# Optimization experiments

Measured on AMD Instinct MI355X. Metric: run time of the kernel, lower is better.

Reference implementation:

```python
import jax, jax.numpy as jnp
import numpy as np

B, S, H, I, E, K = 4, 1024, 1024, 768, 8, 2


def setup_inputs() -> dict:
    key = jax.random.key(0)
    ks = jax.random.split(key, 6)
    return {
        "hidden_states": jax.random.normal(ks[0], (B, S, H), dtype=jnp.float32),
        "routing_weights": jax.random.uniform(ks[1], (B, S, K), dtype=jnp.float32),
        "selected_experts": jax.random.randint(ks[2], (B, S, K), 0, E, dtype=jnp.int64),
        "gate_weight": jax.random.normal(ks[3], (E, I, H), dtype=jnp.float32) * 0.02,
        "up_weight": jax.random.normal(ks[4], (E, I, H), dtype=jnp.float32) * 0.02,
        "down_weight": jax.random.normal(ks[5], (E, H, I), dtype=jnp.float32) * 0.02,
    }


def reference(hidden_states, routing_weights, selected_experts, gate_weight, up_weight, down_weight):
    b, s, h = hidden_states.shape
    x = hidden_states.reshape(-1, h)                    # [T, H]
    T = x.shape[0]
    k = selected_experts.shape[-1]
    rw = routing_weights.astype(x.dtype).reshape(T, k)  # [T, K]
    se = selected_experts.reshape(T, k)                 # [T, K]
    e_total = gate_weight.shape[0]
    # combine[t, e] = sum of routing weights of slots of token t routed to expert e
    # (equivalent to the original per-slot dispatch + weighted scatter-add combine)
    combine = jnp.zeros((T, e_total), dtype=x.dtype).at[jnp.arange(T)[:, None], se].add(rw)
    out = jnp.zeros_like(x)
    for e in range(e_total):  # small fixed expert count
        g = x @ gate_weight[e].T                        # [T, I]
        u = x @ up_weight[e].T                          # [T, I]
        y = (jax.nn.silu(g) * u) @ down_weight[e].T     # [T, H]
        out = out + combine[:, e:e + 1] * y
    return out.reshape(b, s, h)
```

## Files before the change

kernel.cpp:

```cpp
#include <hip/hip_runtime.h>
#include <hip/hip_bf16.h>

typedef __attribute__((ext_vector_type(8))) short bf16x8;
typedef __attribute__((ext_vector_type(4))) float f32x4;

#define T_TOK 4096
#define HDIM  1024
#define IDIM  768
#define NEXP  8
#define TOPK  2
#define NSLOT (T_TOK * TOPK)

#define BM  128
#define BN  64
#define BKS 64

#define NX4 (T_TOK * HDIM / 4)
#define NW4 (NEXP * IDIM * HDIM / 4)

__device__ __forceinline__ ushort f2bf(float f) {
  union { __hip_bfloat16 h; ushort u; } cv;
  cv.h = __float2bfloat16(f);
  return cv.u;
}
__device__ __forceinline__ float bf2f(ushort u) {
  union { float f; uint v; } cv; cv.v = ((uint)u) << 16; return cv.f;
}

__device__ __forceinline__ void gload_lds16(const ushort* g, ushort* l) {
  __builtin_amdgcn_global_load_lds(
      (const __attribute__((address_space(1))) void*)g,
      (__attribute__((address_space(3))) void*)l, 16, 0, 0);
}

__global__ void cvt_all(const float* __restrict__ hs, const float* __restrict__ gw,
                        const float* __restrict__ uw, const float* __restrict__ dw,
                        ushort* __restrict__ xb, ushort* __restrict__ gwb,
                        ushort* __restrict__ uwb, ushort* __restrict__ dwb) {
  int i = blockIdx.x * blockDim.x + threadIdx.x;
  const float* src; ushort* dst; int off;
  if (i < NX4) { src = hs; dst = xb; off = i; }
  else {
    int j = i - NX4;
    if (j < NW4)            { src = gw; dst = gwb; off = j; }
    else if (j < 2 * NW4)   { src = uw; dst = uwb; off = j - NW4; }
    else                    { src = dw; dst = dwb; off = j - 2 * NW4; }
  }
  float4 v = reinterpret_cast<const float4*>(src)[off];
  ushort4 o;
  o.x = f2bf(v.x); o.y = f2bf(v.y); o.z = f2bf(v.z); o.w = f2bf(v.w);
  reinterpret_cast<ushort4*>(dst)[off] = o;
}

__global__ void route_kernel(const int* __restrict__ sel, int* __restrict__ counts,
                             int* __restrict__ toklist) {
  int slot = blockIdx.x * blockDim.x + threadIdx.x;
  if (slot >= NSLOT) return;
  int e = sel[slot];
  int idx = atomicAdd(&counts[e], 1);
  toklist[e * NSLOT + idx] = slot;
}

__launch_bounds__(256, 2)
__global__ void gemm_gateup(const ushort* __restrict__ xb,
                            const ushort* __restrict__ gwb,
                            const ushort* __restrict__ uwb,
                            const int* __restrict__ counts,
                            const int* __restrict__ toklist,
                            ushort* __restrict__ act) {
  const int e = blockIdx.z;
  const int cnt = counts[e];
  const int m0 = blockIdx.y * BM;
  if (m0 >= cnt) return;
  const int n0 = blockIdx.x * BN;

  __shared__ __align__(16) ushort As[2][BM * BKS];
  __shared__ __align__(16) ushort Bgs[2][BN * BKS];
  __shared__ __align__(16) ushort Bus[2][BN * BKS];

  const int tid = threadIdx.x;
  const int wave = tid >> 6, lane = tid & 63;
  const int wm = wave >> 1, wn = wave & 1;
  const int lrow = lane & 15, lk16 = lane >> 4;
  const int rseg = lane >> 3;
  const int ksrc = (lane & 7) ^ rseg;

  int arow[4];
  #pragma unroll
  for (int i = 0; i < 4; ++i) {
    int entry = m0 + wave * 32 + i * 8 + rseg;
    int s = (entry < cnt) ? toklist[e * NSLOT + entry] : 0;
    arow[i] = s >> 1;
  }

  const ushort* gB = gwb + (size_t)e * IDIM * HDIM + (size_t)n0 * HDIM;
  const ushort* uB = uwb + (size_t)e * IDIM * HDIM + (size_t)n0 * HDIM;

  f32x4 accg[4][2], accu[4][2];
  const f32x4 fzero = {0.f, 0.f, 0.f, 0.f};
  #pragma unroll
  for (int a = 0; a < 4; ++a)
    #pragma unroll
    for (int b = 0; b < 2; ++b) { accg[a][b] = fzero; accu[a][b] = fzero; }

  auto stage = [&](int buf, int k0) {
    #pragma unroll
    for (int i = 0; i < 4; ++i) {
      int seg = wave * 4 + i;
      gload_lds16(xb + (size_t)arow[i] * HDIM + k0 + ksrc * 8, &As[buf][seg * 512]);
    }
    #pragma unroll
    for (int i = 0; i < 2; ++i) {
      int seg = wave * 2 + i;
      int br = seg * 8 + rseg;
      gload_lds16(gB + (size_t)br * HDIM + k0 + ksrc * 8, &Bgs[buf][seg * 512]);
      gload_lds16(uB + (size_t)br * HDIM + k0 + ksrc * 8, &Bus[buf][seg * 512]);
    }
  };

  auto compute = [&](int buf) {
    #pragma unroll
    for (int ksub = 0; ksub < 2; ++ksub) {
      bf16x8 aF[4], bgF[2], buF[2];
      const int chunk = ksub * 4 + lk16;
      #pragma unroll
      for (int mi = 0; mi < 4; ++mi) {
        int r = wm * 64 + mi * 16 + lrow;
        aF[mi] = *reinterpret_cast<const bf16x8*>(&As[buf][r * 64 + ((chunk ^ (r & 7)) & 7) * 8]);
      }
      #pragma unroll
      for (int ni = 0; ni < 2; ++ni) {
        int r = wn * 32 + ni * 16 + lrow;
        bgF[ni] = *reinterpret_cast<const bf16x8*>(&Bgs[buf][r * 64 + ((chunk ^ (r & 7)) & 7) * 8]);
        buF[ni] = *reinterpret_cast<const bf16x8*>(&Bus[buf][r * 64 + ((chunk ^ (r & 7)) & 7) * 8]);
      }
      #pragma unroll
      for (int mi = 0; mi < 4; ++mi)
        #pragma unroll
        for (int ni = 0; ni < 2; ++ni) {
          accg[mi][ni] = __builtin_amdgcn_mfma_f32_16x16x32_bf16(aF[mi], bgF[ni], accg[mi][ni], 0, 0, 0);
          accu[mi][ni] = __builtin_amdgcn_mfma_f32_16x16x32_bf16(aF[mi], buF[ni], accu[mi][ni], 0, 0, 0);
        }
    }
  };

  stage(0, 0);
  __syncthreads();
  #pragma unroll 1
  for (int t = 0; t < HDIM / BKS; t += 2) {
    if (t + 1 < HDIM / BKS) stage(1, (t + 1) * BKS);
    compute(0);
    __syncthreads();
    if (t + 2 < HDIM / BKS) stage(0, (t + 2) * BKS);
    compute(1);
    __syncthreads();
  }

  const int lcol = lane & 15;
  const int lrb = (lane >> 4) * 4;
  #pragma unroll
  for (int mi = 0; mi < 4; ++mi)
    #pragma unroll
    for (int j = 0; j < 4; ++j) {
      int row = wm * 64 + mi * 16 + lrb + j;
      int entry = m0 + row;
      if (entry >= cnt) continue;
      int slot = toklist[e * NSLOT + entry];
      #pragma unroll
      for (int ni = 0; ni < 2; ++ni) {
        int col = n0 + wn * 32 + ni * 16 + lcol;
        float g = accg[mi][ni][j];
        float u = accu[mi][ni][j];
        float y = (g / (1.0f + __expf(-g))) * u;
        act[(size_t)slot * IDIM + col] = f2bf(y);
      }
    }
}

__launch_bounds__(256, 3)
__global__ void gemm_down(const ushort* __restrict__ act,
                          const ushort* __restrict__ dwb,
                          const int* __restrict__ counts,
                          const int* __restrict__ toklist,
                          ushort* __restrict__ yact) {
  const int e = blockIdx.z;
  const int cnt = counts[e];
  const int m0 = blockIdx.y * BM;
  if (m0 >= cnt) return;
  const int n0 = blockIdx.x * BN;

  __shared__ __align__(16) ushort As[2][BM * BKS];
  __shared__ __align__(16) ushort Bs[2][BN * BKS];

  const int tid = threadIdx.x;
  const int wave = tid >> 6, lane = tid & 63;
  const int wm = wave >> 1, wn = wave & 1;
  const int lrow = lane & 15, lk16 = lane >> 4;
  const int rseg = lane >> 3;
  const int ksrc = (lane & 7) ^ rseg;

  int arow[4];
  #pragma unroll
  for (int i = 0; i < 4; ++i) {
    int entry = m0 + wave * 32 + i * 8 + rseg;
    arow[i] = (entry < cnt) ? toklist[e * NSLOT + entry] : 0;
  }

  const ushort* dB = dwb + (size_t)e * HDIM * IDIM + (size_t)n0 * IDIM;

  f32x4 acc[4][2];
  const f32x4 fzero = {0.f, 0.f, 0.f, 0.f};
  #pragma unroll
  for (int a = 0; a < 4; ++a)
    #pragma unroll
    for (int b = 0; b < 2; ++b) acc[a][b] = fzero;

  auto stage = [&](int buf, int k0) {
    #pragma unroll
    for (int i = 0; i < 4; ++i) {
      int seg = wave * 4 + i;
      gload_lds16(act + (size_t)arow[i] * IDIM + k0 + ksrc * 8, &As[buf][seg * 512]);
    }
    #pragma unroll
    for (int i = 0; i < 2; ++i) {
      int seg = wave * 2 + i;
      int br = seg * 8 + rseg;
      gload_lds16(dB + (size_t)br * IDIM + k0 + ksrc * 8, &Bs[buf][seg * 512]);
    }
  };

  auto compute = [&](int buf) {
    #pragma unroll
    for (int ksub = 0; ksub < 2; ++ksub) {
      bf16x8 aF[4], bF[2];
      const int chunk = ksub * 4 + lk16;
      #pragma unroll
      for (int mi = 0; mi < 4; ++mi) {
        int r = wm * 64 + mi * 16 + lrow;
        aF[mi] = *reinterpret_cast<const bf16x8*>(&As[buf][r * 64 + ((chunk ^ (r & 7)) & 7) * 8]);
      }
      #pragma unroll
      for (int ni = 0; ni < 2; ++ni) {
        int r = wn * 32 + ni * 16 + lrow;
        bF[ni] = *reinterpret_cast<const bf16x8*>(&Bs[buf][r * 64 + ((chunk ^ (r & 7)) & 7) * 8]);
      }
      #pragma unroll
      for (int mi = 0; mi < 4; ++mi)
        #pragma unroll
        for (int ni = 0; ni < 2; ++ni)
          acc[mi][ni] = __builtin_amdgcn_mfma_f32_16x16x32_bf16(aF[mi], bF[ni], acc[mi][ni], 0, 0, 0);
    }
  };

  stage(0, 0);
  __syncthreads();
  #pragma unroll 1
  for (int t = 0; t < IDIM / BKS; t += 2) {
    if (t + 1 < IDIM / BKS) stage(1, (t + 1) * BKS);
    compute(0);
    __syncthreads();
    if (t + 2 < IDIM / BKS) stage(0, (t + 2) * BKS);
    compute(1);
    __syncthreads();
  }

  const int lcol = lane & 15;
  const int lrb = (lane >> 4) * 4;
  #pragma unroll
  for (int mi = 0; mi < 4; ++mi)
    #pragma unroll
    for (int j = 0; j < 4; ++j) {
      int row = wm * 64 + mi * 16 + lrb + j;
      int entry = m0 + row;
      if (entry >= cnt) continue;
      int slot = toklist[e * NSLOT + entry];
      #pragma unroll
      for (int ni = 0; ni < 2; ++ni) {
        int col = n0 + wn * 32 + ni * 16 + lcol;
        yact[(size_t)slot * HDIM + col] = f2bf(acc[mi][ni][j]);
      }
    }
}

__global__ void combine_kernel(const ushort* __restrict__ yact, const float* __restrict__ rw,
                               float* __restrict__ out) {
  int i = blockIdx.x * blockDim.x + threadIdx.x;
  int t = i >> 7;
  int h0 = (i & 127) << 3;
  const bf16x8 y0 = *reinterpret_cast<const bf16x8*>(yact + (size_t)(2 * t) * HDIM + h0);
  const bf16x8 y1 = *reinterpret_cast<const bf16x8*>(yact + (size_t)(2 * t + 1) * HDIM + h0);
  float w0 = rw[2 * t], w1 = rw[2 * t + 1];
  float o[8];
  #pragma unroll
  for (int j = 0; j < 8; ++j)
    o[j] = w0 * bf2f((ushort)y0[j]) + w1 * bf2f((ushort)y1[j]);
  float4* op = reinterpret_cast<float4*>(out + (size_t)t * HDIM + h0);
  op[0] = make_float4(o[0], o[1], o[2], o[3]);
  op[1] = make_float4(o[4], o[5], o[6], o[7]);
}

extern "C" void kernel_launch(void* const* d_in, const int* in_sizes, int n_in,
                              void* d_out, int out_size, void* d_ws, size_t ws_size,
                              hipStream_t stream) {
  const float* hs = (const float*)d_in[0];
  const float* rw = (const float*)d_in[1];
  const int*   se = (const int*)d_in[2];
  const float* gw = (const float*)d_in[3];
  const float* uw = (const float*)d_in[4];
  const float* dw = (const float*)d_in[5];
  float* out = (float*)d_out;

  char* base = (char*)d_ws;
  ushort* xb      = (ushort*)(base + 0);
  ushort* gwb     = (ushort*)(base + 8388608);
  ushort* uwb     = (ushort*)(base + 20971520);
  ushort* dwb     = (ushort*)(base + 33554432);
  ushort* act     = (ushort*)(base + 46137344);
  ushort* yact    = (ushort*)(base + 8388608);
  int*    toklist = (int*)(base + 58720256);
  int*    counts  = (int*)(base + 58982400);

  hipMemsetAsync(counts, 0, 256, stream);

  int total4 = NX4 + 3 * NW4;
  cvt_all<<<(total4 + 255) / 256, 256, 0, stream>>>(hs, gw, uw, dw, xb, gwb, uwb, dwb);
  route_kernel<<<NSLOT / 256, 256, 0, stream>>>(se, counts, toklist);
  gemm_gateup<<<dim3(IDIM / BN, NSLOT / BM, NEXP), 256, 0, stream>>>(xb, gwb, uwb, counts, toklist, act);
  gemm_down<<<dim3(HDIM / BN, NSLOT / BM, NEXP), 256, 0, stream>>>(act, dwb, counts, toklist, yact);
  combine_kernel<<<T_TOK * HDIM / 8 / 256, 256, 0, stream>>>(yact, rw, out);
}
```

Baseline: 253.1 us.

## Halve K-tile to 32, raise occupancy, and flatten grid with expert-interleaved block order

The K-step of both grouped GEMMs drops from 64 to 32, which halves LDS use per block. Launch bounds rise to 3 and 4 blocks per CU to match. The staging and swizzle are rewritten for 32-wide rows, with one 16-byte load per lane per tile. The 3D grid becomes a 1D grid with the expert as the fastest-varying index, so blocks of different experts run together and the early-exit empty blocks are spread out. The cost is twice as many K iterations and barriers, plus more register pressure from the tighter launch bounds.

```diff
diff --git a/kernel.cpp b/kernel.cpp
--- a/kernel.cpp
+++ b/kernel.cpp
@@ -13,7 +13,7 @@
 
 #define BM  128
 #define BN  64
-#define BKS 64
+#define BKS 32
 
 #define NX4 (T_TOK * HDIM / 4)
 #define NW4 (NEXP * IDIM * HDIM / 4)
@@ -61,18 +61,22 @@
   toklist[e * NSLOT + idx] = slot;
 }
 
-__launch_bounds__(256, 2)
+
+__launch_bounds__(256, 3)
 __global__ void gemm_gateup(const ushort* __restrict__ xb,
                             const ushort* __restrict__ gwb,
                             const ushort* __restrict__ uwb,
                             const int* __restrict__ counts,
                             const int* __restrict__ toklist,
                             ushort* __restrict__ act) {
-  const int e = blockIdx.z;
+  const int b = blockIdx.x;
+  const int e = b & 7;
+  const int r = b >> 3;
+  const int nt = r % 12, mt = r / 12;
   const int cnt = counts[e];
-  const int m0 = blockIdx.y * BM;
+  const int m0 = mt * BM;
   if (m0 >= cnt) return;
-  const int n0 = blockIdx.x * BN;
+  const int n0 = nt * BN;
 
   __shared__ __align__(16) ushort As[2][BM * BKS];
   __shared__ __align__(16) ushort Bgs[2][BN * BKS];
@@ -82,66 +86,55 @@
   const int wave = tid >> 6, lane = tid & 63;
   const int wm = wave >> 1, wn = wave & 1;
   const int lrow = lane & 15, lk16 = lane >> 4;
-  const int rseg = lane >> 3;
-  const int ksrc = (lane & 7) ^ rseg;
-
-  int arow[4];
-  #pragma unroll
-  for (int i = 0; i < 4; ++i) {
-    int entry = m0 + wave * 32 + i * 8 + rseg;
-    int s = (entry < cnt) ? toklist[e * NSLOT + entry] : 0;
-    arow[i] = s >> 1;
-  }
-
-  const ushort* gB = gwb + (size_t)e * IDIM * HDIM + (size_t)n0 * HDIM;
-  const ushort* uB = uwb + (size_t)e * IDIM * HDIM + (size_t)n0 * HDIM;
+  const int rl = lane >> 2;
+  const int gck = ((lane & 3) ^ ((lane >> 3) & 3)) << 3;
+
+  const int ent0 = m0 + wave * 16 + rl;
+  const int ent1 = ent0 + 64;
+  const int arow0 = (ent0 < cnt) ? (toklist[e * NSLOT + ent0] >> 1) : 0;
+  const int arow1 = (ent1 < cnt) ? (toklist[e * NSLOT + ent1] >> 1) : 0;
+  const int brow = wave * 16 + rl;
+
+  const ushort* aP0 = xb + (size_t)arow0 * HDIM + gck;
+  const ushort* aP1 = xb + (size_t)arow1 * HDIM + gck;
+  const ushort* gP = gwb + (size_t)e * IDIM * HDIM + (size_t)(n0 + brow) * HDIM + gck;
+  const ushort* uP = uwb + (size_t)e * IDIM * HDIM + (size_t)(n0 + brow) * HDIM + gck;
 
   f32x4 accg[4][2], accu[4][2];
   const f32x4 fzero = {0.f, 0.f, 0.f, 0.f};
   #pragma unroll
   for (int a = 0; a < 4; ++a)
     #pragma unroll
-    for (int b = 0; b < 2; ++b) { accg[a][b] = fzero; accu[a][b] = fzero; }
+    for (int c = 0; c < 2; ++c) { accg[a][c] = fzero; accu[a][c] = fzero; }
 
   auto stage = [&](int buf, int k0) {
-    #pragma unroll
-    for (int i = 0; i < 4; ++i) {
-      int seg = wave * 4 + i;
-      gload_lds16(xb + (size_t)arow[i] * HDIM + k0 + ksrc * 8, &As[buf][seg * 512]);
-    }
-    #pragma unroll
-    for (int i = 0; i < 2; ++i) {
-      int seg = wave * 2 + i;
-      int br = seg * 8 + rseg;
-      gload_lds16(gB + (size_t)br * HDIM + k0 + ksrc * 8, &Bgs[buf][seg * 512]);
-      gload_lds16(uB + (size_t)br * HDIM + k0 + ksrc * 8, &Bus[buf][seg * 512]);
-    }
+    gload_lds16(aP0 + k0, &As[buf][wave * 512]);
+    gload_lds16(aP1 + k0, &As[buf][(wave + 4) * 512]);
+    gload_lds16(gP + k0, &Bgs[buf][wave * 512]);
+    gload_lds16(uP + k0, &Bus[buf][wave * 512]);
   };
 
+  const int swzc = ((lk16 ^ ((lrow >> 1) & 3)) << 3);
   auto compute = [&](int buf) {
-    #pragma unroll
-    for (int ksub = 0; ksub < 2; ++ksub) {
-      bf16x8 aF[4], bgF[2], buF[2];
-      const int chunk = ksub * 4 + lk16;
-      #pragma unroll
-      for (int mi = 0; mi < 4; ++mi) {
-        int r = wm * 64 + mi * 16 + lrow;
-        aF[mi] = *reinterpret_cast<const bf16x8*>(&As[buf][r * 64 + ((chunk ^ (r & 7)) & 7) * 8]);
-      }
+    bf16x8 aF[4], bgF[2], buF[2];
+    #pragma unroll
+    for (int mi = 0; mi < 4; ++mi) {
+      int rr = wm * 64 + mi * 16 + lrow;
+      aF[mi] = *reinterpret_cast<const bf16x8*>(&As[buf][rr * 32 + swzc]);
+    }
+    #pragma unroll
+    for (int ni = 0; ni < 2; ++ni) {
+      int rr = wn * 32 + ni * 16 + lrow;
+      bgF[ni] = *reinterpret_cast<const bf16x8*>(&Bgs[buf][rr * 32 + swzc]);
+      buF[ni] = *reinterpret_cast<const bf16x8*>(&Bus[buf][rr * 32 + swzc]);
+    }
+    #pragma unroll
+    for (int mi = 0; mi < 4; ++mi)
       #pragma unroll
       for (int ni = 0; ni < 2; ++ni) {
-        int r = wn * 32 + ni * 16 + lrow;
-        bgF[ni] = *reinterpret_cast<const bf16x8*>(&Bgs[buf][r * 64 + ((chunk ^ (r & 7)) & 7) * 8]);
-        buF[ni] = *reinterpret_cast<const bf16x8*>(&Bus[buf][r * 64 + ((chunk ^ (r & 7)) & 7) * 8]);
+        accg[mi][ni] = __builtin_amdgcn_mfma_f32_16x16x32_bf16(aF[mi], bgF[ni], accg[mi][ni], 0, 0, 0);
+        accu[mi][ni] = __builtin_amdgcn_mfma_f32_16x16x32_bf16(aF[mi], buF[ni], accu[mi][ni], 0, 0, 0);
       }
-      #pragma unroll
-      for (int mi = 0; mi < 4; ++mi)
-        #pragma unroll
-        for (int ni = 0; ni < 2; ++ni) {
-          accg[mi][ni] = __builtin_amdgcn_mfma_f32_16x16x32_bf16(aF[mi], bgF[ni], accg[mi][ni], 0, 0, 0);
-          accu[mi][ni] = __builtin_amdgcn_mfma_f32_16x16x32_bf16(aF[mi], buF[ni], accu[mi][ni], 0, 0, 0);
-        }
-    }
   };
 
   stage(0, 0);
@@ -177,17 +170,20 @@
     }
 }
 
-__launch_bounds__(256, 3)
+__launch_bounds__(256, 4)
 __global__ void gemm_down(const ushort* __restrict__ act,
                           const ushort* __restrict__ dwb,
                           const int* __restrict__ counts,
                           const int* __restrict__ toklist,
                           ushort* __restrict__ yact) {
-  const int e = blockIdx.z;
+  const int b = blockIdx.x;
+  const int e = b & 7;
+  const int r = b >> 3;
+  const int nt = r & 15, mt = r >> 4;
   const int cnt = counts[e];
-  const int m0 = blockIdx.y * BM;
+  const int m0 = mt * BM;
   if (m0 >= cnt) return;
-  const int n0 = blockIdx.x * BN;
+  const int n0 = nt * BN;
 
   __shared__ __align__(16) ushort As[2][BM * BKS];
   __shared__ __align__(16) ushort Bs[2][BN * BKS];
@@ -196,60 +192,50 @@
   const int wave = tid >> 6, lane = tid & 63;
   const int wm = wave >> 1, wn = wave & 1;
   const int lrow = lane & 15, lk16 = lane >> 4;
-  const int rseg = lane >> 3;
-  const int ksrc = (lane & 7) ^ rseg;
-
-  int arow[4];
-  #pragma unroll
-  for (int i = 0; i < 4; ++i) {
-    int entry = m0 + wave * 32 + i * 8 + rseg;
-    arow[i] = (entry < cnt) ? toklist[e * NSLOT + entry] : 0;
-  }
-
-  const ushort* dB = dwb + (size_t)e * HDIM * IDIM + (size_t)n0 * IDIM;
+  const int rl = lane >> 2;
+  const int gck = ((lane & 3) ^ ((lane >> 3) & 3)) << 3;
+
+  const int ent0 = m0 + wave * 16 + rl;
+  const int ent1 = ent0 + 64;
+  const int arow0 = (ent0 < cnt) ? toklist[e * NSLOT + ent0] : 0;
+  const int arow1 = (ent1 < cnt) ? toklist[e * NSLOT + ent1] : 0;
+  const int brow = wave * 16 + rl;
+
+  const ushort* aP0 = act + (size_t)arow0 * IDIM + gck;
+  const ushort* aP1 = act + (size_t)arow1 * IDIM + gck;
+  const ushort* dP = dwb + (size_t)e * HDIM * IDIM + (size_t)(n0 + brow) * IDIM + gck;
 
   f32x4 acc[4][2];
   const f32x4 fzero = {0.f, 0.f, 0.f, 0.f};
   #pragma unroll
   for (int a = 0; a < 4; ++a)
     #pragma unroll
-    for (int b = 0; b < 2; ++b) acc[a][b] = fzero;
+    for (int c = 0; c < 2; ++c) acc[a][c] = fzero;
 
   auto stage = [&](int buf, int k0) {
-    #pragma unroll
-    for (int i = 0; i < 4; ++i) {
-      int seg = wave * 4 + i;
-      gload_lds16(act + (size_t)arow[i] * IDIM + k0 + ksrc * 8, &As[buf][seg * 512]);
-    }
-    #pragma unroll
-    for (int i = 0; i < 2; ++i) {
-      int seg = wave * 2 + i;
-      int br = seg * 8 + rseg;
-      gload_lds16(dB + (size_t)br * IDIM + k0 + ksrc * 8, &Bs[buf][seg * 512]);
-    }
+    gload_lds16(aP0 + k0, &As[buf][wave * 512]);
+    gload_lds16(aP1 + k0, &As[buf][(wave + 4) * 512]);
+    gload_lds16(dP + k0, &Bs[buf][wave * 512]);
   };
 
+  const int swzc = ((lk16 ^ ((lrow >> 1) & 3)) << 3);
   auto compute = [&](int buf) {
-    #pragma unroll
-    for (int ksub = 0; ksub < 2; ++ksub) {
-      bf16x8 aF[4], bF[2];
-      const int chunk = ksub * 4 + lk16;
+    bf16x8 aF[4], bF[2];
+    #pragma unroll
+    for (int mi = 0; mi < 4; ++mi) {
+      int rr = wm * 64 + mi * 16 + lrow;
+      aF[mi] = *reinterpret_cast<const bf16x8*>(&As[buf][rr * 32 + swzc]);
+    }
+    #pragma unroll
+    for (int ni = 0; ni < 2; ++ni) {
+      int rr = wn * 32 + ni * 16 + lrow;
+      bF[ni] = *reinterpret_cast<const bf16x8*>(&Bs[buf][rr * 32 + swzc]);
+    }
+    #pragma unroll
+    for (int mi = 0; mi < 4; ++mi)
       #pragma unroll
-      for (int mi = 0; mi < 4; ++mi) {
-        int r = wm * 64 + mi * 16 + lrow;
-        aF[mi] = *reinterpret_cast<const bf16x8*>(&As[buf][r * 64 + ((chunk ^ (r & 7)) & 7) * 8]);
-      }
-      #pragma unroll
-      for (int ni = 0; ni < 2; ++ni) {
-        int r = wn * 32 + ni * 16 + lrow;
-        bF[ni] = *reinterpret_cast<const bf16x8*>(&Bs[buf][r * 64 + ((chunk ^ (r & 7)) & 7) * 8]);
-      }
-      #pragma unroll
-      for (int mi = 0; mi < 4; ++mi)
-        #pragma unroll
-        for (int ni = 0; ni < 2; ++ni)
-          acc[mi][ni] = __builtin_amdgcn_mfma_f32_16x16x32_bf16(aF[mi], bF[ni], acc[mi][ni], 0, 0, 0);
-    }
+      for (int ni = 0; ni < 2; ++ni)
+        acc[mi][ni] = __builtin_amdgcn_mfma_f32_16x16x32_bf16(aF[mi], bF[ni], acc[mi][ni], 0, 0, 0);
   };
 
   stage(0, 0);
@@ -325,7 +311,7 @@
   int total4 = NX4 + 3 * NW4;
   cvt_all<<<(total4 + 255) / 256, 256, 0, stream>>>(hs, gw, uw, dw, xb, gwb, uwb, dwb);
   route_kernel<<<NSLOT / 256, 256, 0, stream>>>(se, counts, toklist);
-  gemm_gateup<<<dim3(IDIM / BN, NSLOT / BM, NEXP), 256, 0, stream>>>(xb, gwb, uwb, counts, toklist, act);
-  gemm_down<<<dim3(HDIM / BN, NSLOT / BM, NEXP), 256, 0, stream>>>(act, dwb, counts, toklist, yact);
+  gemm_gateup<<<8 * 12 * (NSLOT / BM), 256, 0, stream>>>(xb, gwb, uwb, counts, toklist, act);
+  gemm_down<<<8 * 16 * (NSLOT / BM), 256, 0, stream>>>(act, dwb, counts, toklist, yact);
   combine_kernel<<<T_TOK * HDIM / 8 / 256, 256, 0, stream>>>(yact, rw, out);
 }
```

New measurement: 237.2 us. 6.3% less time.
